# Optimization experiments

Hardware: AMD Instinct MI355X
Metric: run time of the kernel (lower is better)

## Reference

```python
import jax, jax.numpy as jnp
import numpy as np

D_MODEL = 1024
N_HEADS = 16
D_HEAD = D_MODEL // N_HEADS


def setup_inputs() -> dict:
    key = jax.random.key(0)
    ks = jax.random.split(key, 9)
    s = 1.0 / np.sqrt(D_MODEL)
    x = jax.random.normal(ks[0], (4, 2048, D_MODEL), dtype=jnp.float32)
    wq = jax.random.uniform(ks[1], (D_MODEL, D_MODEL), jnp.float32, -s, s)
    wk = jax.random.uniform(ks[2], (D_MODEL, D_MODEL), jnp.float32, -s, s)
    wv = jax.random.uniform(ks[3], (D_MODEL, D_MODEL), jnp.float32, -s, s)
    wo = jax.random.uniform(ks[4], (D_MODEL, D_MODEL), jnp.float32, -s, s)
    bq = jax.random.uniform(ks[5], (D_MODEL,), jnp.float32, -s, s)
    bk = jax.random.uniform(ks[6], (D_MODEL,), jnp.float32, -s, s)
    bv = jax.random.uniform(ks[7], (D_MODEL,), jnp.float32, -s, s)
    bo = jax.random.uniform(ks[8], (D_MODEL,), jnp.float32, -s, s)
    return {"x": x, "wq": wq, "bq": bq, "wk": wk, "bk": bk,
            "wv": wv, "bv": bv, "wo": wo, "bo": bo}


def reference(x, wq, bq, wk, bk, wv, bv, wo, bo):
    B, T, D = x.shape
    H, Dh = N_HEADS, D_HEAD
    # nn.Linear: y = x @ W.T + b
    q = (x @ wq.T + bq).reshape(B, T, H, Dh).transpose(0, 2, 1, 3)  # (B,H,T,Dh)
    k = (x @ wk.T + bk).reshape(B, T, H, Dh).transpose(0, 2, 1, 3)
    v = (x @ wv.T + bv).reshape(B, T, H, Dh).transpose(0, 2, 1, 3)
    scores = jnp.einsum('bhqd,bhkd->bhqk', q, k) / jnp.sqrt(jnp.float32(Dh))
    causal_mask = jnp.triu(jnp.ones((T, T), dtype=bool), k=1)  # True above diag
    scores = jnp.where(causal_mask[None, None], jnp.float32(-jnp.inf), scores)
    attn = jax.nn.softmax(scores, axis=-1)  # dropout p=0.0 -> identity
    out = jnp.einsum('bhqk,bhkd->bhqd', attn, v)
    out = out.transpose(0, 2, 1, 3).reshape(B, T, D)
    return out @ wo.T + bo
```

## Files before the change

### kernel.cpp

```cpp
#include <hip/hip_runtime.h>

typedef __bf16 bf16x8 __attribute__((ext_vector_type(8)));
typedef float f32x4 __attribute__((ext_vector_type(4)));
typedef float f32x16 __attribute__((ext_vector_type(16)));
typedef unsigned short u16;
typedef unsigned int u32;

#define DEV static __device__ __forceinline__

DEV u16 f2bf(float f) {
  u32 u = __builtin_bit_cast(u32, f);
  u += 0x7fffu + ((u >> 16) & 1u);
  return (u16)(u >> 16);
}

DEV f32x4 mfma16(bf16x8 a, bf16x8 b, f32x4 c) {
  return __builtin_amdgcn_mfma_f32_16x16x32_bf16(a, b, c, 0, 0, 0);
}

DEV f32x16 mfma32(bf16x8 a, bf16x8 b, f32x16 c) {
  return __builtin_amdgcn_mfma_f32_32x32x16_bf16(a, b, c, 0, 0, 0);
}

DEV u32 cvtpk(float lo, float hi) {
  u32 r;
  asm("v_cvt_pk_bf16_f32 %0, %1, %2" : "=v"(r) : "v"(lo), "v"(hi));
  return r;
}

DEV void gload16(const void* g, void* l) {
  __builtin_amdgcn_global_load_lds((const __attribute__((address_space(1))) u32*)g,
                                   (__attribute__((address_space(3))) u32*)l, 16, 0, 0);
}

__global__ void pack_w(const float* __restrict__ wq, const float* __restrict__ wk,
                       const float* __restrict__ wv, const float* __restrict__ wo,
                       const float* __restrict__ bq, const float* __restrict__ bk,
                       const float* __restrict__ bv,
                       u16* __restrict__ Wqkv, u16* __restrict__ Wo, float* __restrict__ bqkv) {
  const int i = blockIdx.x * 256 + threadIdx.x;
  if (i < 3145728) {
    const int n = i >> 10;
    const float* s = (n < 1024) ? wq : (n < 2048) ? wk : wv;
    Wqkv[i] = f2bf(s[(n & 1023) * 1024 + (i & 1023)]);
  } else if (i < 4194304) {
    Wo[i - 3145728] = f2bf(wo[i - 3145728]);
  } else if (i < 4197376) {
    const int j = i - 4194304;
    bqkv[j] = (j < 1024) ? bq[j] : (j < 2048) ? bk[j - 1024] : bv[j - 2048];
  }
}

__global__ void cvt_x(const float4* __restrict__ x, u16* __restrict__ xb) {
  const int i = blockIdx.x * 256 + threadIdx.x;
  float4 v = x[i];
  union { u16 h[4]; uint2 d; } r;
  r.h[0] = f2bf(v.x); r.h[1] = f2bf(v.y); r.h[2] = f2bf(v.z); r.h[3] = f2bf(v.w);
  *(uint2*)&xb[(size_t)i * 4] = r.d;
}

template<int MODE>
__global__ __launch_bounds__(256)
void gemm_bt(const u16* __restrict__ A, const u16* __restrict__ B,
             const float* __restrict__ bias, float* __restrict__ Cf,
             u16* __restrict__ Qs, u16* __restrict__ Ks, u16* __restrict__ Vts,
             int K) {
  __shared__ u16 Asm[128 * 32];
  __shared__ u16 Bsm[128 * 32];
  const int tid = threadIdx.x, lane = tid & 63, w = tid >> 6;
  const int tn = blockIdx.x, tm = blockIdx.y;
  const int wr = w >> 1, wc = w & 1;
  f32x4 acc[4][4] = {};
  const size_t Kb = (size_t)K * 2;
  const char* Ab = (const char*)A + (size_t)(tm * 128) * Kb;
  const char* Bb = (const char*)B + (size_t)(tn * 128) * Kb;
  const int c0 = w * 2, c1 = c0 + 1;
  const size_t soff0 = (size_t)(c0 * 16 + (lane >> 2)) * Kb + (size_t)(lane & 3) * 16;
  const size_t soff1 = (size_t)(c1 * 16 + (lane >> 2)) * Kb + (size_t)(lane & 3) * 16;
  u16* la0 = Asm + c0 * 512;  u16* la1 = Asm + c1 * 512;
  u16* lb0 = Bsm + c0 * 512;  u16* lb1 = Bsm + c1 * 512;
  const int ar = (wr * 64 + (lane & 15)) * 32 + (lane >> 4) * 8;
  const int br = (wc * 64 + (lane & 15)) * 32 + (lane >> 4) * 8;

  for (int kt = 0; kt < K; kt += 32) {
    if (kt) __syncthreads();
    gload16(Ab + soff0 + (size_t)kt * 2, la0);
    gload16(Ab + soff1 + (size_t)kt * 2, la1);
    gload16(Bb + soff0 + (size_t)kt * 2, lb0);
    gload16(Bb + soff1 + (size_t)kt * 2, lb1);
    __syncthreads();
    bf16x8 af[4], bfv[4];
#pragma unroll
    for (int mf = 0; mf < 4; mf++) af[mf] = *(const bf16x8*)&Asm[ar + mf * 512];
#pragma unroll
    for (int nf = 0; nf < 4; nf++) bfv[nf] = *(const bf16x8*)&Bsm[br + nf * 512];
#pragma unroll
    for (int mf = 0; mf < 4; mf++)
#pragma unroll
      for (int nf = 0; nf < 4; nf++)
        acc[mf][nf] = mfma16(af[mf], bfv[nf], acc[mf][nf]);
  }

  const int nbase = tn * 128 + wc * 64 + (lane & 15);
  const int mbase = tm * 128 + wr * 64 + (lane >> 4) * 4;
  const float SCQ = 0.18033688011112042f;
#pragma unroll
  for (int nf = 0; nf < 4; nf++) {
    const int n = nbase + nf * 16;
    const float bias_n = bias[n];
    if (MODE == 0) {
      const int sec = n >> 10;
      const int h = (n & 1023) >> 6, dh = n & 63;
#pragma unroll
      for (int mf = 0; mf < 4; mf++) {
#pragma unroll
        for (int r = 0; r < 4; r++) {
          const int m = mbase + mf * 16 + r;
          const int b = m >> 11, t = m & 2047;
          const size_t base = (size_t)(b * 16 + h) << 17;
          const float vv = acc[mf][nf][r] + bias_n;
          if (sec == 0)      Qs[base + (size_t)t * 64 + dh] = f2bf(vv * SCQ);
          else if (sec == 1) Ks[base + (size_t)t * 64 + dh] = f2bf(vv);
          else               Vts[base + (size_t)dh * 2048 + t] = f2bf(vv);
        }
      }
    } else {
#pragma unroll
      for (int mf = 0; mf < 4; mf++)
#pragma unroll
        for (int r = 0; r < 4; r++) {
          const int m = mbase + mf * 16 + r;
          Cf[(size_t)m * 1024 + n] = acc[mf][nf][r] + bias_n;
        }
    }
  }
}

__global__ __launch_bounds__(256)
void attn32(const u16* __restrict__ Qg, const u16* __restrict__ Kg,
            const u16* __restrict__ Vt, u16* __restrict__ AO) {
  const int lane = threadIdx.x & 63, w = threadIdx.x >> 6;
  const int bh = blockIdx.x, qt = blockIdx.y;
  const int l31 = lane & 31, h = lane >> 5;
  const int q0 = qt * 128 + w * 32;
  const size_t hb = (size_t)bh << 17;

  bf16x8 qf[4];
  const u16* qrow_p = Qg + hb + (size_t)(q0 + l31) * 64 + h * 8;
#pragma unroll
  for (int s = 0; s < 4; s++) qf[s] = *(const bf16x8*)(qrow_p + s * 16);

  f32x16 o0 = {}, o1 = {};
  float m = -3.0e38f, lr = 0.f;

  const u16* kp  = Kg + hb + (size_t)l31 * 64 + h * 8;
  const u16* vp0 = Vt + hb + (size_t)l31 * 2048 + h * 8;
  const u16* vp1 = Vt + hb + (size_t)(l31 + 32) * 2048 + h * 8;

  for (int kb = 0; kb <= q0; kb += 32) {
    const u16* kt = kp + (size_t)kb * 64;
    bf16x8 kf0 = *(const bf16x8*)(kt);
    bf16x8 kf1 = *(const bf16x8*)(kt + 16);
    bf16x8 kf2 = *(const bf16x8*)(kt + 32);
    bf16x8 kf3 = *(const bf16x8*)(kt + 48);
    f32x16 sa = {};
    sa = mfma32(kf0, qf[0], sa);
    sa = mfma32(kf1, qf[1], sa);
    sa = mfma32(kf2, qf[2], sa);
    sa = mfma32(kf3, qf[3], sa);

    if (kb == q0) {
#pragma unroll
      for (int r = 0; r < 16; r++) {
        const int kl = (r & 3) + 8 * (r >> 2) + 4 * h;
        if (kl > l31) sa[r] = -3.0e38f;
      }
    }

    float pmax = sa[0];
#pragma unroll
    for (int r = 1; r < 16; r++) pmax = fmaxf(pmax, sa[r]);
    pmax = fmaxf(pmax, __shfl_xor(pmax, 32));

    if (!__all(pmax - m <= 8.0f)) {
      const float mn = fmaxf(m, pmax);
      const float al = exp2f(m - mn);
      lr *= al;
#pragma unroll
      for (int r = 0; r < 16; r++) { o0[r] *= al; o1[r] *= al; }
      m = mn;
    }

    float e[16];
    float rs = 0.f;
#pragma unroll
    for (int r = 0; r < 16; r++) { e[r] = exp2f(sa[r] - m); rs += e[r]; }
    rs += __shfl_xor(rs, 32);
    lr += rs;

    u32 W[8];
#pragma unroll
    for (int j = 0; j < 8; j++) W[j] = cvtpk(e[2 * j], e[2 * j + 1]);
    union { u32 u[4]; bf16x8 v; } f0, f1;
    {
      const u32 x0 = __shfl_xor(W[0], 32), x1 = __shfl_xor(W[1], 32);
      const u32 x2 = __shfl_xor(W[2], 32), x3 = __shfl_xor(W[3], 32);
      f0.u[0] = h ? x2 : W[0]; f0.u[1] = h ? x3 : W[1];
      f0.u[2] = h ? W[2] : x0; f0.u[3] = h ? W[3] : x1;
      const u32 y0 = __shfl_xor(W[4], 32), y1 = __shfl_xor(W[5], 32);
      const u32 y2 = __shfl_xor(W[6], 32), y3 = __shfl_xor(W[7], 32);
      f1.u[0] = h ? y2 : W[4]; f1.u[1] = h ? y3 : W[5];
      f1.u[2] = h ? W[6] : y0; f1.u[3] = h ? W[7] : y1;
    }

    bf16x8 v00 = *(const bf16x8*)(vp0 + kb);
    bf16x8 v01 = *(const bf16x8*)(vp0 + kb + 16);
    bf16x8 v10 = *(const bf16x8*)(vp1 + kb);
    bf16x8 v11 = *(const bf16x8*)(vp1 + kb + 16);
    o0 = mfma32(v00, f0.v, o0);
    o0 = mfma32(v01, f1.v, o0);
    o1 = mfma32(v10, f0.v, o1);
    o1 = mfma32(v11, f1.v, o1);
  }

  const float inv = 1.0f / lr;
  const int b = bh >> 4, hh = bh & 15;
  const int q = q0 + l31;
  u16* orow = AO + (size_t)(b * 2048 + q) * 1024 + hh * 64;
#pragma unroll
  for (int r = 0; r < 16; r += 2) {
    const int dh = (r & 3) + 8 * (r >> 2) + 4 * h;
    *(u32*)(orow + dh)      = cvtpk(o0[r] * inv, o0[r + 1] * inv);
    *(u32*)(orow + 32 + dh) = cvtpk(o1[r] * inv, o1[r + 1] * inv);
  }
}

extern "C" void kernel_launch(void* const* d_in, const int* in_sizes, int n_in,
                              void* d_out, int out_size, void* d_ws, size_t ws_size,
                              hipStream_t stream) {
  const float* x  = (const float*)d_in[0];
  const float* wq = (const float*)d_in[1];
  const float* bq = (const float*)d_in[2];
  const float* wk = (const float*)d_in[3];
  const float* bk = (const float*)d_in[4];
  const float* wv = (const float*)d_in[5];
  const float* bv = (const float*)d_in[6];
  const float* wo = (const float*)d_in[7];
  const float* bo = (const float*)d_in[8];

  char* p = (char*)d_ws;
  u16* xb    = (u16*)p;   p += 16777216;
  u16* Wqkv  = (u16*)p;   p += 6291456;
  u16* Wo    = (u16*)p;   p += 2097152;
  float* bqkv = (float*)p; p += 12288;
  u16* Qs    = (u16*)p;   p += 16777216;
  u16* Ks    = (u16*)p;   p += 16777216;
  u16* Vts   = (u16*)p;   p += 16777216;
  u16* AO    = xb;

  pack_w<<<16396, 256, 0, stream>>>(wq, wk, wv, wo, bq, bk, bv, Wqkv, Wo, bqkv);
  cvt_x<<<8192, 256, 0, stream>>>((const float4*)x, xb);
  gemm_bt<0><<<dim3(24, 64), 256, 0, stream>>>(xb, Wqkv, bqkv, nullptr, Qs, Ks, Vts, 1024);
  attn32<<<dim3(64, 16), 256, 0, stream>>>(Qs, Ks, Vts, AO);
  gemm_bt<1><<<dim3(8, 64), 256, 0, stream>>>(AO, Wo, bo, (float*)d_out,
                                              nullptr, nullptr, nullptr, 1024);
}
```

Baseline: 372.6 us.

## Prefetch K tiles, use permlane32 swap, balance causal tiles in attention

The attention kernel now double-buffers its K fragments, loading the next tile while the current one is being processed, and issues the V loads at the start of each step so their latency overlaps the QK MFMAs and the softmax. The shuffle-plus-select exchange of probability fragments is replaced with v_permlane32_swap instructions. The MFMA sections are bracketed with s_setprio, and the query-tile order is remapped so that short and long causal tiles alternate across blocks. Launch bounds now request 4 blocks per CU, which caps register use and could cause spills.

```diff
diff --git a/kernel.cpp b/kernel.cpp
--- a/kernel.cpp
+++ b/kernel.cpp
@@ -136,11 +136,14 @@
   }
 }
 
-__global__ __launch_bounds__(256)
+__global__ __launch_bounds__(256, 4)
 void attn32(const u16* __restrict__ Qg, const u16* __restrict__ Kg,
             const u16* __restrict__ Vt, u16* __restrict__ AO) {
   const int lane = threadIdx.x & 63, w = threadIdx.x >> 6;
-  const int bh = blockIdx.x, qt = blockIdx.y;
+  const int bh = blockIdx.x;
+  const int yy = blockIdx.y;
+  const int gq = yy >> 2, oq = yy & 3;
+  const int qt = (gq == 0) ? oq : (gq == 1) ? 15 - oq : (gq == 2) ? 4 + oq : 11 - oq;
   const int l31 = lane & 31, h = lane >> 5;
   const int q0 = qt * 128 + w * 32;
   const size_t hb = (size_t)bh << 17;
@@ -155,19 +158,31 @@
 
   const u16* kp  = Kg + hb + (size_t)l31 * 64 + h * 8;
   const u16* vp0 = Vt + hb + (size_t)l31 * 2048 + h * 8;
-  const u16* vp1 = Vt + hb + (size_t)(l31 + 32) * 2048 + h * 8;
-
-  for (int kb = 0; kb <= q0; kb += 32) {
-    const u16* kt = kp + (size_t)kb * 64;
-    bf16x8 kf0 = *(const bf16x8*)(kt);
-    bf16x8 kf1 = *(const bf16x8*)(kt + 16);
-    bf16x8 kf2 = *(const bf16x8*)(kt + 32);
-    bf16x8 kf3 = *(const bf16x8*)(kt + 48);
+  const u16* vp1 = vp0 + 32 * 2048;
+
+  bf16x8 kA[4], kB[4];
+#pragma unroll
+  for (int j = 0; j < 4; j++) kA[j] = *(const bf16x8*)(kp + j * 16);
+
+  auto step = [&](bf16x8 (&kc)[4], bf16x8 (&kn)[4], int kb) {
+    bf16x8 vc0 = *(const bf16x8*)(vp0 + kb);
+    bf16x8 vc1 = *(const bf16x8*)(vp0 + kb + 16);
+    bf16x8 vc2 = *(const bf16x8*)(vp1 + kb);
+    bf16x8 vc3 = *(const bf16x8*)(vp1 + kb + 16);
+
     f32x16 sa = {};
-    sa = mfma32(kf0, qf[0], sa);
-    sa = mfma32(kf1, qf[1], sa);
-    sa = mfma32(kf2, qf[2], sa);
-    sa = mfma32(kf3, qf[3], sa);
+    __builtin_amdgcn_s_setprio(1);
+    sa = mfma32(kc[0], qf[0], sa);
+    sa = mfma32(kc[1], qf[1], sa);
+    sa = mfma32(kc[2], qf[2], sa);
+    sa = mfma32(kc[3], qf[3], sa);
+    __builtin_amdgcn_s_setprio(0);
+
+    if (kb + 32 <= q0) {
+      const u16* kt2 = kp + (size_t)(kb + 32) * 64;
+#pragma unroll
+      for (int j = 0; j < 4; j++) kn[j] = *(const bf16x8*)(kt2 + j * 16);
+    }
 
     if (kb == q0) {
 #pragma unroll
@@ -177,9 +192,9 @@
       }
     }
 
-    float pmax = sa[0];
-#pragma unroll
-    for (int r = 1; r < 16; r++) pmax = fmaxf(pmax, sa[r]);
+    float pmax = fmaxf(sa[0], sa[1]);
+#pragma unroll
+    for (int r = 2; r < 16; r++) pmax = fmaxf(pmax, sa[r]);
     pmax = fmaxf(pmax, __shfl_xor(pmax, 32));
 
     if (!__all(pmax - m <= 8.0f)) {
@@ -191,36 +206,40 @@
       m = mn;
     }
 
-    float e[16];
+    u32 W[8];
     float rs = 0.f;
 #pragma unroll
-    for (int r = 0; r < 16; r++) { e[r] = exp2f(sa[r] - m); rs += e[r]; }
+    for (int j = 0; j < 8; j++) {
+      const float e0 = exp2f(sa[2 * j] - m);
+      const float e1 = exp2f(sa[2 * j + 1] - m);
+      rs += e0 + e1;
+      W[j] = cvtpk(e0, e1);
+    }
     rs += __shfl_xor(rs, 32);
     lr += rs;
 
-    u32 W[8];
-#pragma unroll
-    for (int j = 0; j < 8; j++) W[j] = cvtpk(e[2 * j], e[2 * j + 1]);
+    asm volatile("v_permlane32_swap_b32 %0, %1" : "+v"(W[0]), "+v"(W[2]));
+    asm volatile("v_permlane32_swap_b32 %0, %1" : "+v"(W[1]), "+v"(W[3]));
+    asm volatile("v_permlane32_swap_b32 %0, %1" : "+v"(W[4]), "+v"(W[6]));
+    asm volatile("v_permlane32_swap_b32 %0, %1" : "+v"(W[5]), "+v"(W[7]));
     union { u32 u[4]; bf16x8 v; } f0, f1;
-    {
-      const u32 x0 = __shfl_xor(W[0], 32), x1 = __shfl_xor(W[1], 32);
-      const u32 x2 = __shfl_xor(W[2], 32), x3 = __shfl_xor(W[3], 32);
-      f0.u[0] = h ? x2 : W[0]; f0.u[1] = h ? x3 : W[1];
-      f0.u[2] = h ? W[2] : x0; f0.u[3] = h ? W[3] : x1;
-      const u32 y0 = __shfl_xor(W[4], 32), y1 = __shfl_xor(W[5], 32);
-      const u32 y2 = __shfl_xor(W[6], 32), y3 = __shfl_xor(W[7], 32);
-      f1.u[0] = h ? y2 : W[4]; f1.u[1] = h ? y3 : W[5];
-      f1.u[2] = h ? W[6] : y0; f1.u[3] = h ? W[7] : y1;
-    }
-
-    bf16x8 v00 = *(const bf16x8*)(vp0 + kb);
-    bf16x8 v01 = *(const bf16x8*)(vp0 + kb + 16);
-    bf16x8 v10 = *(const bf16x8*)(vp1 + kb);
-    bf16x8 v11 = *(const bf16x8*)(vp1 + kb + 16);
-    o0 = mfma32(v00, f0.v, o0);
-    o0 = mfma32(v01, f1.v, o0);
-    o1 = mfma32(v10, f0.v, o1);
-    o1 = mfma32(v11, f1.v, o1);
+    f0.u[0] = W[0]; f0.u[1] = W[1]; f0.u[2] = W[2]; f0.u[3] = W[3];
+    f1.u[0] = W[4]; f1.u[1] = W[5]; f1.u[2] = W[6]; f1.u[3] = W[7];
+
+    __builtin_amdgcn_s_setprio(1);
+    o0 = mfma32(vc0, f0.v, o0);
+    o0 = mfma32(vc1, f1.v, o0);
+    o1 = mfma32(vc2, f0.v, o1);
+    o1 = mfma32(vc3, f1.v, o1);
+    __builtin_amdgcn_s_setprio(0);
+  };
+
+  int kb = 0;
+  for (;;) {
+    step(kA, kB, kb);
+    kb += 32; if (kb > q0) break;
+    step(kB, kA, kb);
+    kb += 32; if (kb > q0) break;
   }
 
   const float inv = 1.0f / lr;
```

Result: no change. 367.0 us (-1.5%).
